# Kernel tuning notes

Hardware: AMD Instinct MI355X
Metric: run time of the kernel (lower is better)

The kernel has to match this reference:

```python
import jax, jax.numpy as jnp
import numpy as np

BLOCK = 64      # base classifier input height/width
STRIDE = 16     # BLOCK // 4 per Windowing(stride=[1,bh/4,bw/4,1], size=[1,bh,bw,1])
K = 10          # n_classes
THRESH = 0.7    # bbox_threshold


def extract_patches(x):
    # x: [B,H,W,C] -> [B,R,Cc,BLOCK*BLOCK*C], same layout as tf.image.extract_patches
    B, H, Wd, C = x.shape
    R = (H - BLOCK) // STRIDE + 1
    Cc = (Wd - BLOCK) // STRIDE + 1
    rows = jnp.arange(R)[:, None] * STRIDE + jnp.arange(BLOCK)[None, :]   # [R,64]
    cols = jnp.arange(Cc)[:, None] * STRIDE + jnp.arange(BLOCK)[None, :]  # [Cc,64]
    p = x[:, rows]                 # [B,R,64,W,C]
    p = p[:, :, :, cols]           # [B,R,64,Cc,64,C]
    p = jnp.transpose(p, (0, 1, 3, 2, 4, 5))  # [B,R,Cc,64,64,C]
    return p.reshape(B, R, Cc, BLOCK * BLOCK * C)


def connected_components(mask):
    # 4-connected components of a 2D bool mask via iterative min-label propagation.
    # Background = 0; foreground labels are distinct positive ints per component.
    R, C = mask.shape
    big = jnp.int32(R * C + 2)
    init = jnp.where(mask, jnp.arange(1, R * C + 1, dtype=jnp.int32).reshape(R, C), 0)

    def step(lab, _):
        l = jnp.where(mask, lab, big)
        up = jnp.concatenate([jnp.full((1, C), big, l.dtype), l[:-1]], 0)
        dn = jnp.concatenate([l[1:], jnp.full((1, C), big, l.dtype)], 0)
        lf = jnp.concatenate([jnp.full((R, 1), big, l.dtype), l[:, :-1]], 1)
        rt = jnp.concatenate([l[:, 1:], jnp.full((R, 1), big, l.dtype)], 1)
        m = jnp.minimum(jnp.minimum(l, jnp.minimum(up, dn)), jnp.minimum(lf, rt))
        return jnp.where(mask, m, 0), None

    lab, _ = jax.lax.scan(step, init, None, length=2 * (R + C))
    return lab


def boxes_from_labels(lab):
    # Segmented min/max over label ids replaces the per-region python loop:
    # box = [rowmin-1, colmin-1, rowmax+1, colmax+1] per component.
    R, C = lab.shape
    N = R * C
    flat = lab.reshape(N)
    rr = jnp.arange(N, dtype=jnp.int32) // C
    cc = jnp.arange(N, dtype=jnp.int32) % C
    rmin = jax.ops.segment_min(rr, flat, num_segments=N + 1)
    cmin = jax.ops.segment_min(cc, flat, num_segments=N + 1)
    rmax = jax.ops.segment_max(rr, flat, num_segments=N + 1)
    cmax = jax.ops.segment_max(cc, flat, num_segments=N + 1)
    cnt = jax.ops.segment_sum(jnp.ones(N, jnp.int32), flat, num_segments=N + 1)
    valid = (cnt > 0).at[0].set(False)  # slot 0 is background
    boxes = jnp.stack([rmin - 1, cmin - 1, rmax + 1, cmax + 1], -1)
    boxes = jnp.where(valid[:, None], boxes, 0)
    return boxes, valid


def setup_inputs() -> dict:
    key = jax.random.key(0)
    k1, k2, k3 = jax.random.split(key, 3)
    inputs = jax.random.normal(k1, (1, 1024, 1024, 3), dtype=jnp.float32)
    # scale W so logits have ~unit variance -> sparse (realistic) threshold mask
    W = jax.random.normal(k2, (12288, K), dtype=jnp.float32) * 0.01
    b = jax.random.normal(k3, (K,), dtype=jnp.float32)
    return {"inputs": inputs, "W": W, "b": b}


def reference(inputs, W, b):
    patches = extract_patches(inputs)               # [1,R,Cc,D]
    B, R, Cc, D = patches.shape
    logits = patches.reshape(B * R * Cc, D) @ W + b # [N,K]
    prob = jax.nn.softmax(logits, axis=1).reshape(R, Cc, K)
    mask = prob > THRESH                            # [R,Cc,K]
    labels = jax.vmap(connected_components, in_axes=2, out_axes=2)(mask)  # [R,Cc,K]
    boxes, valid = jax.vmap(boxes_from_labels)(jnp.transpose(labels, (2, 0, 1)))
    # boxes: [K, R*Cc+1, 4] padded per-component bboxes; valid: [K, R*Cc+1]
    return prob, labels, boxes, valid
```

## Files before the change

kernel.cpp:

```cpp
#include <hip/hip_runtime.h>
#include <cmath>

#define KCLS 10
#define NCELL 3721
#define BIGV  0x0FFFFFFF

#define OUT_PROB 0
#define OUT_LAB  37210
#define OUT_BOX  74420
#define OUT_VALID 223300

#define DPPADD(x, ctrl) \
    x += __int_as_float(__builtin_amdgcn_update_dpp( \
        0, __float_as_int(x), ctrl, 0xf, 0xf, true))

__device__ __forceinline__ float wave_sum64(float x) {
    DPPADD(x, 0x111);
    DPPADD(x, 0x112);
    DPPADD(x, 0x114);
    DPPADD(x, 0x118);
    DPPADD(x, 0x142);
    DPPADD(x, 0x143);
    return x;
}

__device__ __forceinline__ int swz_fidx(int j) {
    const int row = j / 10;
    const int c   = j - row * 10;
    return (row << 4) + (((c >> 2) ^ ((row >> 1) & 3)) << 2) + (c & 3);
}

__global__ __launch_bounds__(1024) void k1_logits(
    const float* __restrict__ x, const float* __restrict__ W,
    const float* __restrict__ b, float* __restrict__ out)
{
    const int tid  = threadIdx.x;
    const int tsub = tid & 255;
    const int g    = tid >> 8;
    const int wrow = g & 1;
    const int dsl  = g >> 1;
    const int blk  = blockIdx.x;
    const int rg   = blk >> 3;
    const int cg   = blk & 7;

    int r = rg * 2 + wrow; if (r > 60) r = 60;
    const int c0 = (cg == 7) ? 53 : cg * 8;

    __shared__ float  wbuf[2][512 * 16];
    __shared__ float  red[2][2][4][8][KCLS];
    __shared__ double lgs[16][KCLS];

    const int j0 = tid << 2;
    const int d0 = swz_fidx(j0);
    const int d1 = swz_fidx(j0 + 2);
    const int d2 = swz_fidx(4096 + tid);

    const int row = tsub + (dsl << 8);
    const int s3  = (row >> 1) & 3;
    const int rb  = row << 4;
    const int wo0 = rb + ((0 ^ s3) << 2);
    const int wo1 = rb + ((1 ^ s3) << 2);
    const int wo2 = rb + ((2 ^ s3) << 2);

    int i   = row / 192;
    int rem = row - i * 192;
    const float* xb = x + r * 49152 + c0 * 48;

    float acc[8][KCLS];
#pragma unroll
    for (int p = 0; p < 8; ++p)
#pragma unroll
        for (int k = 0; k < KCLS; ++k) acc[p][k] = 0.0f;

    float4 sv; float s1;
    {
        const float4 v0 = *(const float4*)(W + j0);
        const float  v1 = W[4096 + tid];
        float* wb0 = &wbuf[0][0];
        *(float2*)(wb0 + d0) = make_float2(v0.x, v0.y);
        *(float2*)(wb0 + d1) = make_float2(v0.z, v0.w);
        wb0[d2] = v1;
        const float* ws = W + 5120;
        sv = *(const float4*)(ws + j0);
        s1 = ws[4096 + tid];
    }

    for (int it = 0; it < 24; ++it) {
        __syncthreads();
        if (it + 1 < 24) {
            float* wbn = &wbuf[(it + 1) & 1][0];
            *(float2*)(wbn + d0) = make_float2(sv.x, sv.y);
            *(float2*)(wbn + d1) = make_float2(sv.z, sv.w);
            wbn[d2] = s1;
            if (it + 2 < 24) {
                const float* ws = W + (it + 2) * 5120;
                sv = *(const float4*)(ws + j0);
                s1 = ws[4096 + tid];
            }
        }
        const float* wb = &wbuf[it & 1][0];
        const float4 wa  = *(const float4*)(wb + wo0);
        const float4 wbq = *(const float4*)(wb + wo1);
        const float2 wc  = *(const float2*)(wb + wo2);
        const float wv[KCLS] = { wa.x, wa.y, wa.z, wa.w,
                                 wbq.x, wbq.y, wbq.z, wbq.w, wc.x, wc.y };
        const float* xp = xb + i * 3072 + rem;
        float xv[8];
#pragma unroll
        for (int p = 0; p < 8; ++p) xv[p] = xp[p * 48];
#pragma unroll
        for (int p = 0; p < 8; ++p)
#pragma unroll
            for (int k = 0; k < KCLS; ++k) acc[p][k] += xv[p] * wv[k];

        rem += 128; i += 2;
        if (rem >= 192) { rem -= 192; ++i; }
    }

    const int w4 = tsub >> 6;
#pragma unroll
    for (int p = 0; p < 8; ++p)
#pragma unroll
        for (int k = 0; k < KCLS; ++k) {
            const float s = wave_sum64(acc[p][k]);
            if ((tid & 63) == 63) red[wrow][dsl][w4][p][k] = s;
        }
    __syncthreads();

    if (tid < 160) {
        const int wr  = tid / 80;
        const int t80 = tid - wr * 80;
        const int p   = t80 / 10;
        const int kk  = t80 - p * 10;
        double s = (double)b[kk];
#pragma unroll
        for (int ds = 0; ds < 2; ++ds)
#pragma unroll
            for (int w = 0; w < 4; ++w) s += (double)red[wr][ds][w][p][kk];
        lgs[wr * 8 + p][kk] = s;
    }
    __syncthreads();

    if (tid < 16) {
        const int wr = tid >> 3, p = tid & 7;
        const int rr = rg * 2 + wr, cc = c0 + p;
        if (rr <= 60) {
            double l[KCLS];
#pragma unroll
            for (int k = 0; k < KCLS; ++k) l[k] = lgs[tid][k];
            double m = l[0];
#pragma unroll
            for (int k = 1; k < KCLS; ++k) m = fmax(m, l[k]);
            double e[KCLS], ssum = 0.0;
#pragma unroll
            for (int k = 0; k < KCLS; ++k) { e[k] = exp(l[k] - m); ssum += e[k]; }
            const double inv = 1.0 / ssum;
            float* po = out + OUT_PROB + (size_t)(rr * 61 + cc) * KCLS;
#pragma unroll
            for (int k = 0; k < KCLS; ++k) po[k] = (float)(e[k] * inv);
        }
    }
}

__global__ __launch_bounds__(1024) void k2_cc_boxes(float* __restrict__ out)
{
    const int k   = blockIdx.x;
    const int tid = threadIdx.x;

    __shared__ int lab[63 * 64];
    __shared__ int act[NCELL];
    __shared__ int nact, changed;
    __shared__ int rmn[NCELL + 1], rmx[NCELL + 1], cmn[NCELL + 1], cmx[NCELL + 1];

    for (int idx = tid; idx < 63 * 64; idx += 1024) lab[idx] = BIGV;
    for (int s = tid; s <= NCELL; s += 1024) {
        rmn[s] = 0x7fffffff; cmn[s] = 0x7fffffff; rmx[s] = -1; cmx[s] = -1;
    }
    if (tid == 0) nact = 0;
    __syncthreads();

    for (int idx = tid; idx < NCELL; idx += 1024) {
        const float pv = out[OUT_PROB + (size_t)idx * KCLS + k];
        if (pv > 0.7f) {
            const int r = idx / 61, c = idx - r * 61;
            const int off = (r + 1) * 64 + (c + 1);
            lab[off] = off;
            act[atomicAdd(&nact, 1)] = off;
        }
    }
    __syncthreads();
    const int na = nact;

    for (int round = 0; round < 128; ++round) {
        if (tid == 0) changed = 0;
        __syncthreads();
        bool ch = false;
        for (int ii = tid; ii < na; ii += 1024) {
            const int off = act[ii];
            const int v = lab[off];
            int m = v, t;
            t = lab[off - 1];  if (t < m) m = t;
            t = lab[off + 1];  if (t < m) m = t;
            t = lab[off - 64]; if (t < m) m = t;
            t = lab[off + 64]; if (t < m) m = t;
            if (m < v) {
                int p = lab[m];
                while (p < m) { m = p; p = lab[m]; }
                atomicMin(&lab[off], m);
                atomicMin(&lab[v],   m);
                ch = true;
            }
        }
        if (ch) changed = 1;
        __syncthreads();
        if (changed == 0) break;
        __syncthreads();
    }

    for (int idx = tid; idx < NCELL; idx += 1024) {
        const int r = idx / 61, c = idx - r * 61;
        const int v = lab[(r + 1) * 64 + (c + 1)];
        const int lv = (v < BIGV) ? ((v >> 6) * 61 - 61 + (v & 63)) : 0;
        out[OUT_LAB + (size_t)idx * KCLS + k] = (float)lv;
    }

    for (int ii = tid; ii < na; ii += 1024) {
        const int off = act[ii];
        const int v = lab[off];
        const int lb = (v >> 6) * 61 - 61 + (v & 63);
        const int r = (off >> 6) - 1, c = (off & 63) - 1;
        atomicMin(&rmn[lb], r); atomicMax(&rmx[lb], r);
        atomicMin(&cmn[lb], c); atomicMax(&cmx[lb], c);
    }
    __syncthreads();

    for (int s = tid; s <= NCELL; s += 1024) {
        const bool val = (s > 0) && (rmx[s] >= 0);
        float* bo = out + OUT_BOX + (size_t)(k * (NCELL + 1) + s) * 4;
        if (val) {
            bo[0] = (float)(rmn[s] - 1);
            bo[1] = (float)(cmn[s] - 1);
            bo[2] = (float)(rmx[s] + 1);
            bo[3] = (float)(cmx[s] + 1);
        } else {
            bo[0] = 0.0f; bo[1] = 0.0f; bo[2] = 0.0f; bo[3] = 0.0f;
        }
        out[OUT_VALID + (size_t)k * (NCELL + 1) + s] = val ? 1.0f : 0.0f;
    }
}

extern "C" void kernel_launch(void* const* d_in, const int* in_sizes, int n_in,
                              void* d_out, int out_size, void* d_ws, size_t ws_size,
                              hipStream_t stream) {
    const float* x = (const float*)d_in[0];
    const float* W = (const float*)d_in[1];
    const float* b = (const float*)d_in[2];
    float* out = (float*)d_out;

    k1_logits  <<<dim3(248), dim3(1024), 0, stream>>>(x, W, b, out);
    k2_cc_boxes<<<dim3(KCLS), dim3(1024), 0, stream>>>(out);
}
```

Measured before the change: 91.95 us.

## Split logits work across class halves with smaller blocks and more grid parallelism

The logits kernel now gives each block one patch row and 8 columns using 512 threads. The two 256-thread halves each compute 5 of the 10 classes over the full 768-row D slice, across 48 iterations instead of 24. This halves per-thread accumulators (80 down to 40 registers), which allows higher occupancy, and doubles the grid to 488 blocks to fill more CUs. In exchange, each x element is loaded twice (once per class half), there are more barriers per block, and the W staging buffer is smaller, so more iterations are needed.

```diff
diff --git a/kernel.cpp b/kernel.cpp
--- a/kernel.cpp
+++ b/kernel.cpp
@@ -30,135 +30,131 @@
     return (row << 4) + (((c >> 2) ^ ((row >> 1) & 3)) << 2) + (c & 3);
 }
 
-__global__ __launch_bounds__(1024) void k1_logits(
+__global__ __launch_bounds__(512, 4) void k1_logits(
     const float* __restrict__ x, const float* __restrict__ W,
     const float* __restrict__ b, float* __restrict__ out)
 {
     const int tid  = threadIdx.x;
     const int tsub = tid & 255;
-    const int g    = tid >> 8;
-    const int wrow = g & 1;
-    const int dsl  = g >> 1;
-    const int blk  = blockIdx.x;
-    const int rg   = blk >> 3;
-    const int cg   = blk & 7;
-
-    int r = rg * 2 + wrow; if (r > 60) r = 60;
-    const int c0 = (cg == 7) ? 53 : cg * 8;
-
-    __shared__ float  wbuf[2][512 * 16];
-    __shared__ float  red[2][2][4][8][KCLS];
-    __shared__ double lgs[16][KCLS];
+    const int kh   = tid >> 8;
+    const int r    = blockIdx.x >> 3;
+    const int cg   = blockIdx.x & 7;
+    const int c0   = (cg == 7) ? 53 : cg * 8;
+
+    __shared__ float  wbuf[2][256 * 16];
+    __shared__ float  red[8][8][5];
+    __shared__ double lgs[8][KCLS];
 
     const int j0 = tid << 2;
     const int d0 = swz_fidx(j0);
     const int d1 = swz_fidx(j0 + 2);
-    const int d2 = swz_fidx(4096 + tid);
-
-    const int row = tsub + (dsl << 8);
-    const int s3  = (row >> 1) & 3;
-    const int rb  = row << 4;
-    const int wo0 = rb + ((0 ^ s3) << 2);
-    const int wo1 = rb + ((1 ^ s3) << 2);
-    const int wo2 = rb + ((2 ^ s3) << 2);
-
-    int i   = row / 192;
-    int rem = row - i * 192;
+    const int je = 2048 + tid;
+    const int d2 = swz_fidx(je);
+
+    const int s3 = (tsub >> 1) & 3;
+    const int rb = tsub << 4;
+    const int q0 = rb + ((0 ^ s3) << 2);
+    const int q1 = rb + ((1 ^ s3) << 2);
+    const int q2 = rb + ((2 ^ s3) << 2);
+
+    int i   = (tsub >= 192) ? 1 : 0;
+    int rem = tsub - i * 192;
     const float* xb = x + r * 49152 + c0 * 48;
 
-    float acc[8][KCLS];
+    float acc[8][5];
 #pragma unroll
     for (int p = 0; p < 8; ++p)
 #pragma unroll
-        for (int k = 0; k < KCLS; ++k) acc[p][k] = 0.0f;
+        for (int k = 0; k < 5; ++k) acc[p][k] = 0.0f;
 
     float4 sv; float s1;
     {
         const float4 v0 = *(const float4*)(W + j0);
-        const float  v1 = W[4096 + tid];
+        const float  v1 = W[je];
         float* wb0 = &wbuf[0][0];
         *(float2*)(wb0 + d0) = make_float2(v0.x, v0.y);
         *(float2*)(wb0 + d1) = make_float2(v0.z, v0.w);
         wb0[d2] = v1;
-        const float* ws = W + 5120;
+        const float* ws = W + 2560;
         sv = *(const float4*)(ws + j0);
-        s1 = ws[4096 + tid];
-    }
-
-    for (int it = 0; it < 24; ++it) {
-        __syncthreads();
-        if (it + 1 < 24) {
+        s1 = ws[je];
+    }
+
+    for (int it = 0; it < 48; ++it) {
+        __syncthreads();
+        if (it + 1 < 48) {
             float* wbn = &wbuf[(it + 1) & 1][0];
             *(float2*)(wbn + d0) = make_float2(sv.x, sv.y);
             *(float2*)(wbn + d1) = make_float2(sv.z, sv.w);
             wbn[d2] = s1;
-            if (it + 2 < 24) {
-                const float* ws = W + (it + 2) * 5120;
+            if (it + 2 < 48) {
+                const float* ws = W + (it + 2) * 2560;
                 sv = *(const float4*)(ws + j0);
-                s1 = ws[4096 + tid];
+                s1 = ws[je];
             }
         }
-        const float* wb = &wbuf[it & 1][0];
-        const float4 wa  = *(const float4*)(wb + wo0);
-        const float4 wbq = *(const float4*)(wb + wo1);
-        const float2 wc  = *(const float2*)(wb + wo2);
-        const float wv[KCLS] = { wa.x, wa.y, wa.z, wa.w,
-                                 wbq.x, wbq.y, wbq.z, wbq.w, wc.x, wc.y };
         const float* xp = xb + i * 3072 + rem;
         float xv[8];
 #pragma unroll
         for (int p = 0; p < 8; ++p) xv[p] = xp[p * 48];
+
+        const float* wb = &wbuf[it & 1][0];
+        float wv[5];
+        if (kh == 0) {
+            const float4 a = *(const float4*)(wb + q0);
+            wv[0] = a.x; wv[1] = a.y; wv[2] = a.z; wv[3] = a.w;
+            wv[4] = wb[q1];
+        } else {
+            const float4 a = *(const float4*)(wb + q1);
+            const float2 c = *(const float2*)(wb + q2);
+            wv[0] = a.y; wv[1] = a.z; wv[2] = a.w; wv[3] = c.x; wv[4] = c.y;
+        }
 #pragma unroll
         for (int p = 0; p < 8; ++p)
 #pragma unroll
-            for (int k = 0; k < KCLS; ++k) acc[p][k] += xv[p] * wv[k];
-
-        rem += 128; i += 2;
+            for (int k = 0; k < 5; ++k) acc[p][k] += xv[p] * wv[k];
+
+        rem += 64; ++i;
         if (rem >= 192) { rem -= 192; ++i; }
     }
 
-    const int w4 = tsub >> 6;
+    const int w = tid >> 6;
 #pragma unroll
     for (int p = 0; p < 8; ++p)
 #pragma unroll
-        for (int k = 0; k < KCLS; ++k) {
+        for (int k = 0; k < 5; ++k) {
             const float s = wave_sum64(acc[p][k]);
-            if ((tid & 63) == 63) red[wrow][dsl][w4][p][k] = s;
-        }
-    __syncthreads();
-
-    if (tid < 160) {
-        const int wr  = tid / 80;
-        const int t80 = tid - wr * 80;
-        const int p   = t80 / 10;
-        const int kk  = t80 - p * 10;
+            if ((tid & 63) == 63) red[w][p][k] = s;
+        }
+    __syncthreads();
+
+    if (tid < 80) {
+        const int p  = tid / 10;
+        const int kk = tid - p * 10;
+        const int khk = (kk >= 5) ? 1 : 0;
+        const int k5  = kk - khk * 5;
         double s = (double)b[kk];
 #pragma unroll
-        for (int ds = 0; ds < 2; ++ds)
-#pragma unroll
-            for (int w = 0; w < 4; ++w) s += (double)red[wr][ds][w][p][kk];
-        lgs[wr * 8 + p][kk] = s;
-    }
-    __syncthreads();
-
-    if (tid < 16) {
-        const int wr = tid >> 3, p = tid & 7;
-        const int rr = rg * 2 + wr, cc = c0 + p;
-        if (rr <= 60) {
-            double l[KCLS];
-#pragma unroll
-            for (int k = 0; k < KCLS; ++k) l[k] = lgs[tid][k];
-            double m = l[0];
-#pragma unroll
-            for (int k = 1; k < KCLS; ++k) m = fmax(m, l[k]);
-            double e[KCLS], ssum = 0.0;
-#pragma unroll
-            for (int k = 0; k < KCLS; ++k) { e[k] = exp(l[k] - m); ssum += e[k]; }
-            const double inv = 1.0 / ssum;
-            float* po = out + OUT_PROB + (size_t)(rr * 61 + cc) * KCLS;
-#pragma unroll
-            for (int k = 0; k < KCLS; ++k) po[k] = (float)(e[k] * inv);
-        }
+        for (int j = 0; j < 4; ++j) s += (double)red[khk * 4 + j][p][k5];
+        lgs[p][kk] = s;
+    }
+    __syncthreads();
+
+    if (tid < 8) {
+        const int cc = c0 + tid;
+        double l[KCLS];
+#pragma unroll
+        for (int k = 0; k < KCLS; ++k) l[k] = lgs[tid][k];
+        double m = l[0];
+#pragma unroll
+        for (int k = 1; k < KCLS; ++k) m = fmax(m, l[k]);
+        double e[KCLS], ssum = 0.0;
+#pragma unroll
+        for (int k = 0; k < KCLS; ++k) { e[k] = exp(l[k] - m); ssum += e[k]; }
+        const double inv = 1.0 / ssum;
+        float* po = out + OUT_PROB + (size_t)(r * 61 + cc) * KCLS;
+#pragma unroll
+        for (int k = 0; k < KCLS; ++k) po[k] = (float)(e[k] * inv);
     }
 }
 
@@ -257,6 +253,6 @@
     const float* b = (const float*)d_in[2];
     float* out = (float*)d_out;
 
-    k1_logits  <<<dim3(248), dim3(1024), 0, stream>>>(x, W, b, out);
+    k1_logits  <<<dim3(488), dim3(512), 0, stream>>>(x, W, b, out);
     k2_cc_boxes<<<dim3(KCLS), dim3(1024), 0, stream>>>(out);
 }
```

New measurement: 101.5 us. +10.4%, slower.
